# Kernel tuning notes

Hardware: AMD Instinct MI355X
Metric: run time of the kernel (lower is better)

The kernel has to match this reference:

```python
import jax, jax.numpy as jnp
import numpy as np

N = 40000      # num_ent
INIT = 100     # init_dim
D = 200        # gcn_dim
F = 4          # num_factors
E = 800000     # num edges (incl. inverses)
NREL = 800     # num_rel * 2
L = 2          # gcn_layer
B = 2048       # batch of (sub, rel)
H2 = D // 2    # CLUBSample hidden_size // 2
NPAIR = F * (F - 1) // 2  # 6 MI discriminators


def setup_inputs() -> dict:
    key = jax.random.key(0)
    ks = jax.random.split(key, 24)
    inp = {}
    inp['sub'] = jax.random.randint(ks[0], (B,), 0, N)
    inp['rel'] = jax.random.randint(ks[1], (B,), 0, NREL)
    inp['edge_index'] = jax.random.randint(ks[2], (2, E), 0, N)
    inp['edge_type'] = jax.random.randint(ks[3], (E,), 0, NREL)
    inp['perm'] = jax.random.permutation(ks[4], B)
    s = 0.05
    inp['init_embed'] = jax.random.normal(ks[5], (N, INIT), jnp.float32) * s
    inp['init_rel'] = jax.random.normal(ks[6], (NREL, D), jnp.float32) * s
    stdv = 1.0 / np.sqrt(F * D)
    inp['pca_w'] = jax.random.uniform(ks[7], (INIT, F * D), jnp.float32, -stdv, stdv)
    inp['pca_b'] = jax.random.uniform(ks[8], (F * D,), jnp.float32, -stdv, stdv)
    inp['cw_w'] = jax.random.normal(ks[9], (D, D), jnp.float32) * 0.1
    inp['w_rel'] = jax.random.normal(ks[10], (L, D, D), jnp.float32) * s
    # CLUBSample MLPs stacked over the NPAIR discriminators
    inp['mu_w1'] = jax.random.normal(ks[11], (NPAIR, D, H2), jnp.float32) * s
    inp['mu_b1'] = jnp.zeros((NPAIR, H2), jnp.float32)
    inp['mu_w2'] = jax.random.normal(ks[12], (NPAIR, H2, D), jnp.float32) * s
    inp['mu_b2'] = jnp.zeros((NPAIR, D), jnp.float32)
    inp['lv_w1'] = jax.random.normal(ks[13], (NPAIR, D, H2), jnp.float32) * s
    inp['lv_b1'] = jnp.zeros((NPAIR, H2), jnp.float32)
    inp['lv_w2'] = jax.random.normal(ks[14], (NPAIR, H2, D), jnp.float32) * s
    inp['lv_b2'] = jnp.zeros((NPAIR, D), jnp.float32)
    return inp


def _leaky(v):
    return jnp.where(v > 0, v, 0.2 * v)


def _club(xi, yj, yj_perm, w1, b1, w2, b2, v1, c1, v2, c2):
    # CLUBSample.forward: MI upper bound between factor i and factor j
    mu = jax.nn.relu(xi @ w1 + b1) @ w2 + b2
    logvar = jnp.tanh(jax.nn.relu(xi @ v1 + c1) @ v2 + c2)
    inv_var = jnp.exp(-logvar)
    pos = -(mu - yj) ** 2 * inv_var
    neg = -(mu - yj_perm) ** 2 * inv_var
    return (pos.sum(-1) - neg.sum(-1)).mean() / 2.0


def _encode(init_embed, init_rel, pca_w, pca_b, cw_w, w_rel, edge_index, edge_type):
    # SparseInputLinear + tanh -> [N, F, D]
    x = jnp.tanh(init_embed @ pca_w + pca_b).reshape(N, F, D)
    # CalculateWeight: leaky_relu matmul then softmax over the factor axis
    kw = _leaky(x.reshape(-1, D) @ cw_w).reshape(N, F, D)
    kw = jax.nn.softmax(kw, axis=1)
    r = init_rel
    src, dst = edge_index[0], edge_index[1]
    for l in range(L):
        r_edge = r[edge_type]  # [E, D]
        aggs = []
        for k in range(F):  # small fixed loop over factors to bound memory
            m = x[src, k] * r_edge                              # [E, D] messages
            logit = _leaky(jnp.sum(m * x[dst, k], axis=-1))     # [E] attention logits
            mx = jax.ops.segment_max(logit, dst, num_segments=N)
            a = jnp.exp(logit - mx[dst])
            den = jax.ops.segment_sum(a, dst, num_segments=N)
            a = a / (den[dst] + 1e-16)                          # per-dst softmax
            aggs.append(jax.ops.segment_sum(a[:, None] * m, dst, num_segments=N))
        agg = jnp.stack(aggs, axis=1)                           # [N, F, D]
        x = jnp.tanh(agg) * kw                                  # factor routing
        r = r @ w_rel[l]
    return x, r


def reference(sub, rel, edge_index, edge_type, perm,
              init_embed, init_rel, pca_w, pca_b, cw_w, w_rel,
              mu_w1, mu_b1, mu_w2, mu_b2, lv_w1, lv_b1, lv_w2, lv_b2):
    x, _ = _encode(init_embed, init_rel, pca_w, pca_b, cw_w, w_rel, edge_index, edge_type)
    sub_emb = x[sub].reshape(B, F * D)
    rel_emb = jnp.tile(init_rel[rel], (1, F))  # index_select + repeat(1, F)
    mi_loss = jnp.float32(0.0)
    cnt = 0
    for i in range(F):
        for j in range(i + 1, F):
            xi = sub_emb[:, i * D:(i + 1) * D]
            yj = sub_emb[:, j * D:(j + 1) * D]
            mi_loss = mi_loss + _club(xi, yj, yj[perm],
                                      mu_w1[cnt], mu_b1[cnt], mu_w2[cnt], mu_b2[cnt],
                                      lv_w1[cnt], lv_b1[cnt], lv_w2[cnt], lv_b2[cnt])
            cnt += 1
    return (sub_emb, rel_emb, x, mi_loss)
```

## Files before the change

kernel.cpp:

```cpp
#include <hip/hip_runtime.h>
#include <hip/hip_bf16.h>

#define N_NODES 40000
#define INIT_D  100
#define DD      200
#define FF      4
#define EE      800000
#define NRELS   800
#define BB      2048
#define H2D     100
#define FD      800
#define RPAD    224
#define XPAD    256

typedef __hip_bfloat16 bf16;
typedef unsigned char u8;
typedef unsigned short u16;
typedef unsigned int u32;
typedef float floatx2 __attribute__((ext_vector_type(2)));
typedef float floatx4 __attribute__((ext_vector_type(4)));
typedef u32 u32x2 __attribute__((ext_vector_type(2)));
typedef short bshort8 __attribute__((ext_vector_type(8)));

#define XSCALE 256.f
#define XINV   (1.f / 256.f)

__device__ __forceinline__ float b2f(bf16 v) { return __bfloat162float(v); }

__device__ __forceinline__ void fp8x4_dec(u32 q, float* o) {
    floatx2 lo = __builtin_amdgcn_cvt_pk_f32_fp8((int)q, false);
    floatx2 hi = __builtin_amdgcn_cvt_pk_f32_fp8((int)q, true);
    o[0] = lo.x; o[1] = lo.y; o[2] = hi.x; o[3] = hi.y;
}

__device__ __forceinline__ u32 fp8x4_enc(float v0, float v1, float v2, float v3) {
    int o = 0;
    o = __builtin_amdgcn_cvt_pk_fp8_f32(v0, v1, o, false);
    o = __builtin_amdgcn_cvt_pk_fp8_f32(v2, v3, o, true);
    return (u32)o;
}

__device__ __forceinline__ float red16(float v) {
    int t;
    t = __builtin_amdgcn_update_dpp(0, __float_as_int(v), 0xB1, 0xF, 0xF, true);
    v += __int_as_float(t);
    t = __builtin_amdgcn_update_dpp(0, __float_as_int(v), 0x4E, 0xF, 0xF, true);
    v += __int_as_float(t);
    t = __builtin_amdgcn_update_dpp(0, __float_as_int(v), 0x124, 0xF, 0xF, true);
    v += __int_as_float(t);
    t = __builtin_amdgcn_update_dpp(0, __float_as_int(v), 0x128, 0xF, 0xF, true);
    v += __int_as_float(t);
    return v;
}

__device__ __forceinline__ bshort8 fp8x8_bf16(u32x2 q) {
    float f[8];
    fp8x4_dec(q.x, f); fp8x4_dec(q.y, f + 4);
    bshort8 r;
#pragma unroll
    for (int j = 0; j < 8; j++) r[j] = (short)(__float_as_uint(f[j]) >> 16);
    return r;
}

__global__ __launch_bounds__(256) void zero_kernel(int* count, double* loss, u8* pad0, u8* pad1) {
    int idx = blockIdx.x * 256 + threadIdx.x;
    if (idx < N_NODES) count[idx] = 0;
    if (idx == 0) *loss = 0.0;
    if (idx < 64 && pad0) ((u32*)pad0)[idx] = 0u;
    if (idx < 64 && pad1) ((u32*)pad1)[idx] = 0u;
}

__global__ __launch_bounds__(64) void pca_kernel(const float* __restrict__ emb,
                                                 const float* __restrict__ pw,
                                                 const float* __restrict__ pb,
                                                 u8* __restrict__ xq,
                                                 float* __restrict__ xf,
                                                 int mode) {
    __shared__ float es[INIT_D][18];
    int r0 = blockIdx.y * 16;
    int c  = blockIdx.x * 64 + threadIdx.x;
    for (int idx = threadIdx.x; idx < 16 * INIT_D; idx += 64) {
        int r = idx / INIT_D, k = idx % INIT_D;
        es[k][r] = emb[(size_t)(r0 + r) * INIT_D + k];
    }
    __syncthreads();
    if (c >= FD) return;
    floatx2 acc[8];
#pragma unroll
    for (int i = 0; i < 8; i++) acc[i] = (floatx2){0.f, 0.f};
    for (int k = 0; k < INIT_D; k++) {
        float w = pw[k * FD + c];
        floatx2 w2 = (floatx2){w, w};
#pragma unroll
        for (int i = 0; i < 8; i++) acc[i] += *(const floatx2*)&es[k][2 * i] * w2;
    }
    float bias = pb[c];
#pragma unroll
    for (int r = 0; r < 16; r++) {
        float a = (r & 1) ? acc[r >> 1].y : acc[r >> 1].x;
        float v = tanhf(a + bias);
        if (mode == 0) {
            int t8 = __builtin_amdgcn_cvt_pk_fp8_f32(v * XSCALE, 0.f, 0, false);
            xq[(size_t)(r0 + r) * FD + c] = (u8)(t8 & 0xFF);
        } else {
            xf[(size_t)(r0 + r) * FD + c] = v;
        }
    }
}

__global__ __launch_bounds__(256) void bpack_kernel(const float* __restrict__ cw,
                                                    u16* __restrict__ bpH,
                                                    u16* __restrict__ bpL) {
    int w = (blockIdx.x * 256 + threadIdx.x) >> 6;
    int lane = threadIdx.x & 63;
    if (w >= 91) return;
    int t = w / 7, s = w % 7;
    int col = t * 16 + (lane & 15);
    int g = lane >> 4;
    bshort8 hv, lv;
#pragma unroll
    for (int j = 0; j < 8; j++) {
        int k = s * 32 + g * 8 + j;
        float v = (k < DD && col < DD) ? cw[k * DD + col] : 0.f;
        u32 b = __float_as_uint(v);
        u32 rb = b + 0x7FFFu + ((b >> 16) & 1u);
        u16 h = (u16)(rb >> 16);
        float hf = __uint_as_float(((u32)h) << 16);
        float lo = v - hf;
        u32 lb = __float_as_uint(lo);
        lb += 0x7FFFu + ((lb >> 16) & 1u);
        hv[j] = (short)h;
        lv[j] = (short)(lb >> 16);
    }
    size_t base = ((size_t)w * 64 + lane) * 8;
    *(bshort8*)(bpH + base) = hv;
    *(bshort8*)(bpL + base) = lv;
}

__global__ __launch_bounds__(256) void kw_mfma(const u8* __restrict__ xq,
                                               const u16* __restrict__ bpH,
                                               const u16* __restrict__ bpL,
                                               u8* __restrict__ kwout) {
    int wv = threadIdx.x >> 6, lane = threadIdx.x & 63;
    int Mbase = blockIdx.x * 128 + wv * 32;
    int g = lane >> 4, c16 = lane & 15;
    floatx4 acc[2][13];
#pragma unroll
    for (int m = 0; m < 2; m++)
#pragma unroll
        for (int t = 0; t < 13; t++) acc[m][t] = (floatx4){0.f, 0.f, 0.f, 0.f};

    const u8* a0p = xq + (size_t)(Mbase + c16) * DD + g * 8;
    const u8* a1p = a0p + 16 * DD;

    for (int s = 0; s < 7; s++) {
        u32x2 qa = *(const u32x2*)(a0p + s * 32);
        u32x2 qb = *(const u32x2*)(a1p + s * 32);
        bshort8 a0 = fp8x8_bf16(qa);
        bshort8 a1 = fp8x8_bf16(qb);
        const u16* hp = bpH + s * 512 + lane * 8;
        const u16* lp = bpL + s * 512 + lane * 8;
#pragma unroll
        for (int t = 0; t < 13; t++) {
            bshort8 bh = *(const bshort8*)(hp + (size_t)t * 3584);
            bshort8 bl = *(const bshort8*)(lp + (size_t)t * 3584);
            acc[0][t] = __builtin_amdgcn_mfma_f32_16x16x32_bf16(a0, bh, acc[0][t], 0, 0, 0);
            acc[1][t] = __builtin_amdgcn_mfma_f32_16x16x32_bf16(a1, bh, acc[1][t], 0, 0, 0);
            acc[0][t] = __builtin_amdgcn_mfma_f32_16x16x32_bf16(a0, bl, acc[0][t], 0, 0, 0);
            acc[1][t] = __builtin_amdgcn_mfma_f32_16x16x32_bf16(a1, bl, acc[1][t], 0, 0, 0);
        }
    }

    int rq = g * 4;
#pragma unroll
    for (int m = 0; m < 2; m++) {
#pragma unroll
        for (int t = 0; t < 13; t++) {
            int col = t * 16 + c16;
            if (col >= DD) continue;
            floatx4 a = acc[m][t];
            float v0 = a.x * XINV, v1 = a.y * XINV, v2 = a.z * XINV, v3 = a.w * XINV;
            v0 = v0 > 0.f ? v0 : 0.2f * v0;
            v1 = v1 > 0.f ? v1 : 0.2f * v1;
            v2 = v2 > 0.f ? v2 : 0.2f * v2;
            v3 = v3 > 0.f ? v3 : 0.2f * v3;
            float mx = fmaxf(fmaxf(v0, v1), fmaxf(v2, v3));
            float e0 = __expf(v0 - mx), e1 = __expf(v1 - mx);
            float e2 = __expf(v2 - mx), e3 = __expf(v3 - mx);
            float inv = 1.f / (e0 + e1 + e2 + e3);
            size_t base = (size_t)(Mbase + m * 16 + rq) * DD + col;
            kwout[base]           = (u8)(e0 * inv * 255.f + 0.5f);
            kwout[base + DD]      = (u8)(e1 * inv * 255.f + 0.5f);
            kwout[base + 2 * DD]  = (u8)(e2 * inv * 255.f + 0.5f);
            kwout[base + 3 * DD]  = (u8)(e3 * inv * 255.f + 0.5f);
        }
    }
}

__global__ __launch_bounds__(256) void kw_old(const float* __restrict__ x,
                                              const float* __restrict__ cw,
                                              u8* __restrict__ kw) {
    int wave = threadIdx.x >> 6, lane = threadIdx.x & 63;
    int n = blockIdx.x * 4 + wave;
    const float* xp = x + (size_t)n * FD;
    float acc[4][4];
#pragma unroll
    for (int f = 0; f < 4; f++)
#pragma unroll
        for (int i = 0; i < 4; i++) acc[f][i] = 0.f;
    for (int k = 0; k < DD; k++) {
        float xv0 = xp[k], xv1 = xp[DD + k];
        float xv2 = xp[2 * DD + k], xv3 = xp[3 * DD + k];
#pragma unroll
        for (int i = 0; i < 4; i++) {
            int d = i * 64 + lane;
            float w = (d < DD) ? cw[k * DD + d] : 0.f;
            acc[0][i] += xv0 * w; acc[1][i] += xv1 * w;
            acc[2][i] += xv2 * w; acc[3][i] += xv3 * w;
        }
    }
    u8* kwp = kw + (size_t)n * FD;
#pragma unroll
    for (int i = 0; i < 4; i++) {
        int d = i * 64 + lane;
        if (d >= DD) continue;
        float v0 = acc[0][i], v1 = acc[1][i], v2 = acc[2][i], v3 = acc[3][i];
        v0 = v0 > 0.f ? v0 : 0.2f * v0;
        v1 = v1 > 0.f ? v1 : 0.2f * v1;
        v2 = v2 > 0.f ? v2 : 0.2f * v2;
        v3 = v3 > 0.f ? v3 : 0.2f * v3;
        float m = fmaxf(fmaxf(v0, v1), fmaxf(v2, v3));
        float e0 = __expf(v0 - m), e1 = __expf(v1 - m), e2 = __expf(v2 - m), e3 = __expf(v3 - m);
        float inv = 1.f / (e0 + e1 + e2 + e3);
        kwp[d]          = (u8)(e0 * inv * 255.f + 0.5f);
        kwp[DD + d]     = (u8)(e1 * inv * 255.f + 0.5f);
        kwp[2 * DD + d] = (u8)(e2 * inv * 255.f + 0.5f);
        kwp[3 * DD + d] = (u8)(e3 * inv * 255.f + 0.5f);
    }
}

__global__ __launch_bounds__(256) void count_kernel(const int* __restrict__ dst, int* count) {
    int e = blockIdx.x * 256 + threadIdx.x;
    atomicAdd(&count[dst[e]], 1);
}

__global__ __launch_bounds__(1024) void scan_kernel(int* __restrict__ count, int* __restrict__ offs) {
    __shared__ int wsums[16];
    __shared__ int carry_s;
    int tid = threadIdx.x;
    int wv = tid >> 6, lane = tid & 63;
    if (tid == 0) { carry_s = 0; offs[0] = 0; }
    __syncthreads();
    for (int base = 0; base < 40960; base += 1024) {
        int i = base + tid;
        int v = (i < N_NODES) ? count[i] : 0;
        if (i < N_NODES) count[i] = 0;
        int x = v;
#pragma unroll
        for (int off = 1; off < 64; off <<= 1) {
            int y = __shfl_up(x, off, 64);
            if (lane >= off) x += y;
        }
        if (lane == 63) wsums[wv] = x;
        __syncthreads();
        if (wv == 0) {
            int s = (lane < 16) ? wsums[lane] : 0;
#pragma unroll
            for (int off = 1; off < 16; off <<= 1) {
                int y = __shfl_up(s, off, 64);
                if (lane >= off) s += y;
            }
            if (lane < 16) wsums[lane] = s;
        }
        __syncthreads();
        int add = carry_s + (wv > 0 ? wsums[wv - 1] : 0);
        int incl = x + add;
        if (i < N_NODES) offs[i + 1] = incl;
        __syncthreads();
        if (tid == 1023) carry_s = incl;
        __syncthreads();
    }
}

__global__ __launch_bounds__(256) void scatter_kernel(const int* __restrict__ src,
                                                      const int* __restrict__ dst,
                                                      const int* __restrict__ etyp,
                                                      const int* __restrict__ offs,
                                                      int* cursor,
                                                      u32* __restrict__ ep) {
    int e = blockIdx.x * 256 + threadIdx.x;
    int d = dst[e];
    int p = offs[d] + atomicAdd(&cursor[d], 1);
    ep[p] = ((u32)etyp[e] << 16) | (u32)src[e];
}

__global__ __launch_bounds__(256) void r0pad_kernel(const float* __restrict__ r0,
                                                    float* __restrict__ rp) {
    int idx = blockIdx.x * 256 + threadIdx.x;
    int n = idx / RPAD, d = idx % RPAD;
    rp[idx] = (d < DD) ? r0[n * DD + d] : 0.f;
}

__global__ __launch_bounds__(256) void rmul_kernel(const float* __restrict__ r0,
                                                   const float* __restrict__ w,
                                                   float* __restrict__ r1) {
    __shared__ float row[DD];
    int n = blockIdx.x;
    if (threadIdx.x < DD) row[threadIdx.x] = r0[n * DD + threadIdx.x];
    __syncthreads();
    int d = threadIdx.x;
    if (d < DD) {
        float acc = 0.f;
        for (int k = 0; k < DD; k++) acc += row[k] * w[k * DD + d];
        r1[n * RPAD + d] = acc;
    } else if (d < RPAD) {
        r1[n * RPAD + d] = 0.f;
    }
}

__global__ __launch_bounds__(256) void agg_fp8(const u8* __restrict__ xin,
                                               const u8* __restrict__ kwv,
                                               const float* __restrict__ r,
                                               const int* __restrict__ offs,
                                               const u32* __restrict__ ep,
                                               u8* __restrict__ xoq,
                                               float* __restrict__ xof,
                                               int mode) {
    int n    = blockIdx.x * 4 + (threadIdx.x >> 6);
    int lane = threadIdx.x & 63;
    int f    = lane >> 4;
    int k    = lane & 15;
    bool act = k < 13;
    int xoff = f * DD + k * 16;
    int roffc = k * 16; if (roffc > 200) roffc = 200;

    float xdf[16];
    {
        const u8* xdp = xin + (size_t)n * FD + xoff;
        u32x2 a = *(const u32x2*)xdp;
        u32x2 b = *(const u32x2*)(xdp + 8);
        fp8x4_dec(a.x, xdf); fp8x4_dec(a.y, xdf + 4);
        fp8x4_dec(b.x, xdf + 8); fp8x4_dec(b.y, xdf + 12);
    }
    floatx2 xd2[8];
#pragma unroll
    for (int j = 0; j < 8; j++) xd2[j] = (floatx2){xdf[2 * j], xdf[2 * j + 1]};

    floatx2 A[8];
#pragma unroll
    for (int j = 0; j < 8; j++) A[j] = (floatx2){0.f, 0.f};
    float Sm = 0.f;

    int e0 = offs[n], e1 = offs[n + 1];

#define ISSUE(QA, QB, R0, R1, R2, R3, JJ) do {                                  \
    u32 wrd_ = (u32)__builtin_amdgcn_readlane((int)epv, (JJ));                  \
    int s_ = (int)(wrd_ & 0xFFFFu), t_ = (int)(wrd_ >> 16);                     \
    const u8* xsp_ = xin + (size_t)s_ * FD;                                     \
    const float* rp_ = r + (size_t)t_ * RPAD + roffc;                           \
    QA = *(const u32x2*)(xsp_ + xoff);                                          \
    QB = *(const u32x2*)(xsp_ + xoff + 8);                                      \
    const floatx4* r4_ = (const floatx4*)rp_;                                   \
    R0 = r4_[0]; R1 = r4_[1]; R2 = r4_[2]; R3 = r4_[3];                         \
} while (0)

#define COMPUTE(QA, QB, R0, R1, R2, R3) do {                                    \
    float xsf_[16];                                                             \
    fp8x4_dec(QA.x, xsf_);     fp8x4_dec(QA.y, xsf_ + 4);                       \
    fp8x4_dec(QB.x, xsf_ + 8); fp8x4_dec(QB.y, xsf_ + 12);                      \
    floatx2 rr_[8];                                                             \
    rr_[0] = (floatx2){R0.x, R0.y}; rr_[1] = (floatx2){R0.z, R0.w};             \
    rr_[2] = (floatx2){R1.x, R1.y}; rr_[3] = (floatx2){R1.z, R1.w};             \
    rr_[4] = (floatx2){R2.x, R2.y}; rr_[5] = (floatx2){R2.z, R2.w};             \
    rr_[6] = (floatx2){R3.x, R3.y}; rr_[7] = (floatx2){R3.z, R3.w};             \
    floatx2 mm_[8];                                                             \
    floatx2 ps_ = (floatx2){0.f, 0.f};                                          \
    _Pragma("unroll")                                                           \
    for (int j_ = 0; j_ < 8; j_++) {                                            \
        floatx2 xs2_ = (floatx2){xsf_[2 * j_], xsf_[2 * j_ + 1]};               \
        mm_[j_] = xs2_ * rr_[j_];                                               \
        ps_ += mm_[j_] * xd2[j_];                                               \
    }                                                                           \
    float p_ = red16(ps_.x + ps_.y);                                            \
    float q_ = p_ * (XINV * XINV);                                              \
    float lg_ = fmaxf(q_, 0.2f * q_);                                           \
    float wg_ = __expf(lg_);                                                    \
    Sm += wg_;                                                                  \
    floatx2 w2_ = (floatx2){wg_, wg_};                                          \
    _Pragma("unroll")                                                           \
    for (int j_ = 0; j_ < 8; j_++) A[j_] += w2_ * mm_[j_];                      \
} while (0)

    for (int cb = e0; cb < e1; cb += 64) {
        int cnt = e1 - cb; if (cnt > 64) cnt = 64;
        u32 epv = ep[cb + (lane < cnt ? lane : cnt - 1)];
        u32x2 qaA, qbA, qaB, qbB;
        floatx4 rA0, rA1, rA2, rA3, rB0, rB1, rB2, rB3;
        ISSUE(qaA, qbA, rA0, rA1, rA2, rA3, 0);
        if (cnt > 1) ISSUE(qaB, qbB, rB0, rB1, rB2, rB3, 1);
        int m2 = cnt & ~1;
        for (int ii = 0; ii < m2; ii += 2) {
            COMPUTE(qaA, qbA, rA0, rA1, rA2, rA3);
            if (ii + 2 < cnt) ISSUE(qaA, qbA, rA0, rA1, rA2, rA3, ii + 2);
            COMPUTE(qaB, qbB, rB0, rB1, rB2, rB3);
            if (ii + 3 < cnt) ISSUE(qaB, qbB, rB0, rB1, rB2, rB3, ii + 3);
        }
        if (cnt & 1) COMPUTE(qaA, qbA, rA0, rA1, rA2, rA3);
    }
#undef ISSUE
#undef COMPUTE

    float inv = 1.f / (Sm + 1e-16f);
    u32 kws[4];
    {
        const u8* kwp = kwv + (size_t)n * FD + xoff;
        u32x2 ka = *(const u32x2*)kwp;
        u32x2 kb = *(const u32x2*)(kwp + 8);
        kws[0] = ka.x; kws[1] = ka.y; kws[2] = kb.x; kws[3] = kb.y;
    }
    float v[16];
#pragma unroll
    for (int j = 0; j < 16; j++) {
        float kv = (float)((kws[j >> 2] >> ((j & 3) * 8)) & 0xFF) * (1.f / 255.f);
        float Aj = (j & 1) ? A[j >> 1].y : A[j >> 1].x;
        v[j] = tanhf(Aj * inv * XINV) * kv;
    }
    if (mode == 0) {
        if (act) {
            u32 o0 = fp8x4_enc(v[0] * XSCALE, v[1] * XSCALE, v[2] * XSCALE, v[3] * XSCALE);
            u32 o1 = fp8x4_enc(v[4] * XSCALE, v[5] * XSCALE, v[6] * XSCALE, v[7] * XSCALE);
            u32 o2 = fp8x4_enc(v[8] * XSCALE, v[9] * XSCALE, v[10] * XSCALE, v[11] * XSCALE);
            u32 o3 = fp8x4_enc(v[12] * XSCALE, v[13] * XSCALE, v[14] * XSCALE, v[15] * XSCALE);
            u8* op = xoq + (size_t)n * FD + xoff;
            *(u32x2*)op = (u32x2){o0, o1};
            if (k < 12) *(u32x2*)(op + 8) = (u32x2){o2, o3};
        }
    } else {
        if (act) {
            float* op = xof + (size_t)n * FD + xoff;
            *(floatx4*)op       = (floatx4){v[0], v[1], v[2], v[3]};
            *(floatx4*)(op + 4) = (floatx4){v[4], v[5], v[6], v[7]};
            if (k < 12) {
                *(floatx4*)(op + 8)  = (floatx4){v[8], v[9], v[10], v[11]};
                *(floatx4*)(op + 12) = (floatx4){v[12], v[13], v[14], v[15]};
            }
        }
    }
}

__global__ __launch_bounds__(256) void agg_sliced(const float* __restrict__ xall,
                                                  const u8* __restrict__ kw,
                                                  const float* __restrict__ r,
                                                  const int* __restrict__ offs,
                                                  const u32* __restrict__ ep,
                                                  bf16* __restrict__ xtmp,
                                                  int f) {
    int n    = blockIdx.x * 4 + (threadIdx.x >> 6);
    int lane = threadIdx.x & 63;
    const float* xdp = xall + (size_t)n * FD + f * DD;
    float xd[4];
#pragma unroll
    for (int i = 0; i < 4; i++) {
        int d = i * 64 + lane;
        xd[i] = (d < DD) ? xdp[d] : 0.f;
    }
    float M = -INFINITY, S = 0.f;
    float A0 = 0.f, A1 = 0.f, A2 = 0.f, A3 = 0.f;
    int e0 = offs[n], e1 = offs[n + 1];
    for (int e = e0; e < e1; ++e) {
        u32 wrd = ep[e];
        int s = wrd & 0xFFFF, t = wrd >> 16;
        const float* xsp = xall + (size_t)s * FD + f * DD;
        const float* rp = r + (size_t)t * RPAD;
        float mm[4];
        float p = 0.f;
#pragma unroll
        for (int i = 0; i < 4; i++) {
            int d = i * 64 + lane;
            float xs = (d < DD) ? xsp[d] : 0.f;
            float rrv = (d < DD) ? rp[d] : 0.f;
            mm[i] = xs * rrv;
            p += mm[i] * xd[i];
        }
#pragma unroll
        for (int o = 32; o > 0; o >>= 1) p += __shfl_xor(p, o, 64);
        float logit = p > 0.f ? p : 0.2f * p;
        float nm = fmaxf(M, logit);
        float sc = __expf(M - nm);
        float w  = __expf(logit - nm);
        S  = S * sc + w;
        A0 = A0 * sc + w * mm[0];
        A1 = A1 * sc + w * mm[1];
        A2 = A2 * sc + w * mm[2];
        A3 = A3 * sc + w * mm[3];
        M = nm;
    }
    float inv = 1.f / (S + 1e-16f);
    const u8* kwp = kw + (size_t)n * FD + f * DD;
    bf16* xo = xtmp + (size_t)n * DD;
    float A[4] = {A0, A1, A2, A3};
#pragma unroll
    for (int i = 0; i < 4; i++) {
        int d = i * 64 + lane;
        if (d < DD) {
            float kv = (float)kwp[d] * (1.f / 255.f);
            xo[d] = __float2bfloat16(tanhf(A[i] * inv) * kv);
        }
    }
}

__global__ __launch_bounds__(256) void copyback_kernel(const bf16* __restrict__ xtmp,
                                                       float* __restrict__ xall, int f) {
    int idx = blockIdx.x * 256 + threadIdx.x;
    int n = idx / DD, d = idx % DD;
    xall[(size_t)n * FD + f * DD + d] = b2f(xtmp[idx]);
}

__global__ __launch_bounds__(256) void subemb_kernel(const float* __restrict__ x,
                                                     const int* __restrict__ sub,
                                                     float* __restrict__ out) {
    int idx = blockIdx.x * 256 + threadIdx.x;
    int b = idx / FD, c = idx % FD;
    out[idx] = x[(size_t)sub[b] * FD + c];
}

__global__ __launch_bounds__(256) void relemb_kernel(const float* __restrict__ ir,
                                                     const int* __restrict__ rel,
                                                     float* __restrict__ out) {
    int idx = blockIdx.x * 256 + threadIdx.x;
    int b = idx / FD, d = idx % DD;
    out[idx] = ir[(size_t)rel[b] * DD + d];
}

__global__ __launch_bounds__(256) void club_kernel(const float* __restrict__ se,
                                                   const int* __restrict__ perm,
                                                   const float* __restrict__ mu_w1, const float* __restrict__ mu_b1,
                                                   const float* __restrict__ mu_w2, const float* __restrict__ mu_b2,
                                                   const float* __restrict__ lv_w1, const float* __restrict__ lv_b1,
                                                   const float* __restrict__ lv_w2, const float* __restrict__ lv_b2,
                                                   double* loss) {
    const int PI[6] = {0, 0, 0, 1, 1, 2};
    const int PJ[6] = {1, 2, 3, 2, 3, 3};
    int p = blockIdx.y;
    int i = PI[p], j = PJ[p];
    __shared__ float xi[DD], yj[DD], yjp[DD], h1m[H2D], h1v[H2D];
    __shared__ float wsum[4];
    float psum = 0.f;
    for (int rr = 0; rr < 8; ++rr) {
        int b = blockIdx.x * 8 + rr;
        int bp = perm[b];
        if (threadIdx.x < DD) {
            int t = threadIdx.x;
            xi[t]  = se[(size_t)b * FD + i * DD + t];
            yj[t]  = se[(size_t)b * FD + j * DD + t];
            yjp[t] = se[(size_t)bp * FD + j * DD + t];
        }
        __syncthreads();
        if (threadIdx.x < H2D) {
            int c = threadIdx.x;
            float a1 = mu_b1[p * H2D + c];
            float a2 = lv_b1[p * H2D + c];
            for (int d = 0; d < DD; d++) {
                float xv = xi[d];
                a1 += xv * mu_w1[(size_t)p * DD * H2D + d * H2D + c];
                a2 += xv * lv_w1[(size_t)p * DD * H2D + d * H2D + c];
            }
            h1m[c] = fmaxf(a1, 0.f);
            h1v[c] = fmaxf(a2, 0.f);
        }
        __syncthreads();
        if (threadIdx.x < DD) {
            int d = threadIdx.x;
            float m = mu_b2[p * DD + d];
            float v = lv_b2[p * DD + d];
            for (int c = 0; c < H2D; c++) {
                m += h1m[c] * mu_w2[(size_t)p * H2D * DD + c * DD + d];
                v += h1v[c] * lv_w2[(size_t)p * H2D * DD + c * DD + d];
            }
            float lv = tanhf(v);
            float ivr = __expf(-lv);
            float d1 = m - yj[d], d2 = m - yjp[d];
            psum += (d2 * d2 - d1 * d1) * ivr;
        }
        __syncthreads();
    }
    float v = psum;
#pragma unroll
    for (int o = 32; o > 0; o >>= 1) v += __shfl_xor(v, o, 64);
    if ((threadIdx.x & 63) == 0) wsum[threadIdx.x >> 6] = v;
    __syncthreads();
    if (threadIdx.x == 0) {
        double t = (double)wsum[0] + (double)wsum[1] + (double)wsum[2] + (double)wsum[3];
        atomicAdd(loss, t / (2.0 * (double)BB));
    }
}

__global__ void loss_out_kernel(const double* loss, float* out) {
    if (threadIdx.x == 0 && blockIdx.x == 0)
        out[0] = (float)(*loss);
}

extern "C" void kernel_launch(void* const* d_in, const int* in_sizes, int n_in,
                              void* d_out, int out_size, void* d_ws, size_t ws_size,
                              hipStream_t stream) {
    const int* sub  = (const int*)d_in[0];
    const int* rel  = (const int*)d_in[1];
    const int* eidx = (const int*)d_in[2];
    const int* etyp = (const int*)d_in[3];
    const int* perm = (const int*)d_in[4];
    const float* init_embed = (const float*)d_in[5];
    const float* init_rel   = (const float*)d_in[6];
    const float* pca_w = (const float*)d_in[7];
    const float* pca_b = (const float*)d_in[8];
    const float* cw_w  = (const float*)d_in[9];
    const float* w_rel = (const float*)d_in[10];
    const float* mu_w1 = (const float*)d_in[11];
    const float* mu_b1 = (const float*)d_in[12];
    const float* mu_w2 = (const float*)d_in[13];
    const float* mu_b2 = (const float*)d_in[14];
    const float* lv_w1 = (const float*)d_in[15];
    const float* lv_b1 = (const float*)d_in[16];
    const float* lv_w2 = (const float*)d_in[17];
    const float* lv_b2 = (const float*)d_in[18];

    float* out = (float*)d_out;
    const size_t OFF_SUB = 0;
    const size_t OFF_REL = 1638400;
    const size_t OFF_X   = 3276800;
    const size_t OFF_MI  = 35276800;
    float* xall = out + OFF_X;

    const int* src = eidx;
    const int* dst = eidx + EE;

    bool fast = (ws_size >= (size_t)101 * 1000 * 1000);

    char* w = (char*)d_ws;
    u8* xq0 = nullptr; u8* xq1 = nullptr; bf16* xtmp = nullptr;
    if (fast) {
        xq0 = (u8*)w; w += (size_t)N_NODES * FD + XPAD;
        xq1 = (u8*)w; w += (size_t)N_NODES * FD + XPAD;
    } else {
        xtmp = (bf16*)w; w += (size_t)N_NODES * DD * 2;
    }
    u8*   kwb  = (u8*)w;    w += (size_t)N_NODES * FD + XPAD;
    float* r0p = (float*)w; w += NRELS * RPAD * 4;
    float* r1  = (float*)w; w += NRELS * RPAD * 4;
    u32* ep    = (u32*)w;   w += EE * 4;
    int* count = (int*)w;   w += N_NODES * 4;
    int* offs  = (int*)w;   w += (N_NODES + 16) * 4;
    double* loss = (double*)w; w += 256;

    u16* bpH = (u16*)ep;
    u16* bpL = bpH + 13 * 7 * 64 * 8;

    hipLaunchKernelGGL(zero_kernel, dim3(157), dim3(256), 0, stream, count, loss,
                       fast ? xq0 + (size_t)N_NODES * FD : nullptr,
                       fast ? xq1 + (size_t)N_NODES * FD : nullptr);
    if (fast) hipLaunchKernelGGL(bpack_kernel, dim3(23), dim3(256), 0, stream, cw_w, bpH, bpL);
    hipLaunchKernelGGL(pca_kernel, dim3(13, 2500), dim3(64), 0, stream,
                       init_embed, pca_w, pca_b, xq0, xall, fast ? 0 : 1);
    if (fast) hipLaunchKernelGGL(kw_mfma, dim3(1250), dim3(256), 0, stream, xq0, bpH, bpL, kwb);
    else      hipLaunchKernelGGL(kw_old, dim3(10000), dim3(256), 0, stream, xall, cw_w, kwb);
    hipLaunchKernelGGL(count_kernel, dim3(3125), dim3(256), 0, stream, dst, count);
    hipLaunchKernelGGL(scan_kernel, dim3(1), dim3(1024), 0, stream, count, offs);
    hipLaunchKernelGGL(scatter_kernel, dim3(3125), dim3(256), 0, stream, src, dst, etyp, offs, count, ep);
    hipLaunchKernelGGL(r0pad_kernel, dim3(700), dim3(256), 0, stream, init_rel, r0p);
    hipLaunchKernelGGL(rmul_kernel, dim3(800), dim3(256), 0, stream, init_rel, w_rel, r1);

    if (fast) {
        hipLaunchKernelGGL(agg_fp8, dim3(10000), dim3(256), 0, stream,
                           xq0, kwb, r0p, offs, ep, xq1, (float*)nullptr, 0);
        hipLaunchKernelGGL(agg_fp8, dim3(10000), dim3(256), 0, stream,
                           xq1, kwb, r1, offs, ep, (u8*)nullptr, xall, 1);
    } else {
        for (int f = 0; f < FF; f++) {
            hipLaunchKernelGGL(agg_sliced, dim3(10000), dim3(256), 0, stream,
                               xall, kwb, r0p, offs, ep, xtmp, f);
            hipLaunchKernelGGL(copyback_kernel, dim3(31250), dim3(256), 0, stream, xtmp, xall, f);
        }
        for (int f = 0; f < FF; f++) {
            hipLaunchKernelGGL(agg_sliced, dim3(10000), dim3(256), 0, stream,
                               xall, kwb, r1, offs, ep, xtmp, f);
            hipLaunchKernelGGL(copyback_kernel, dim3(31250), dim3(256), 0, stream, xtmp, xall, f);
        }
    }

    hipLaunchKernelGGL(subemb_kernel, dim3(6400), dim3(256), 0, stream, xall, sub, out + OFF_SUB);
    hipLaunchKernelGGL(relemb_kernel, dim3(6400), dim3(256), 0, stream, init_rel, rel, out + OFF_REL);
    hipLaunchKernelGGL(club_kernel, dim3(256, 6), dim3(256), 0, stream, out + OFF_SUB, perm,
                       mu_w1, mu_b1, mu_w2, mu_b2, lv_w1, lv_b1, lv_w2, lv_b2, loss);
    hipLaunchKernelGGL(loss_out_kernel, dim3(1), dim3(64), 0, stream, loss, out + OFF_MI);
}
```

Before: 1.215 ms.

## Sort nodes by degree, stage B in LDS, deepen agg pipeline, rebalance CLUB

After: 1.412 ms. 16.2% more time.

```diff
diff --git a/kernel.cpp b/kernel.cpp
--- a/kernel.cpp
+++ b/kernel.cpp
@@ -62,12 +62,14 @@
     return r;
 }
 
-__global__ __launch_bounds__(256) void zero_kernel(int* count, double* loss, u8* pad0, u8* pad1) {
+__global__ __launch_bounds__(256) void zero_kernel(int* count, double* loss, u8* pad0, u8* pad1,
+                                                   int* bins, int* bcur) {
     int idx = blockIdx.x * 256 + threadIdx.x;
     if (idx < N_NODES) count[idx] = 0;
     if (idx == 0) *loss = 0.0;
     if (idx < 64 && pad0) ((u32*)pad0)[idx] = 0u;
     if (idx < 64 && pad1) ((u32*)pad1)[idx] = 0u;
+    if (idx < 256 && bins) { bins[idx] = 0; bcur[idx] = 0; }
 }
 
 __global__ __launch_bounds__(64) void pca_kernel(const float* __restrict__ emb,
@@ -109,8 +111,7 @@
 }
 
 __global__ __launch_bounds__(256) void bpack_kernel(const float* __restrict__ cw,
-                                                    u16* __restrict__ bpH,
-                                                    u16* __restrict__ bpL) {
+                                                    u16* __restrict__ bp) {
     int w = (blockIdx.x * 256 + threadIdx.x) >> 6;
     int lane = threadIdx.x & 63;
     if (w >= 91) return;
@@ -132,15 +133,15 @@
         hv[j] = (short)h;
         lv[j] = (short)(lb >> 16);
     }
-    size_t base = ((size_t)w * 64 + lane) * 8;
-    *(bshort8*)(bpH + base) = hv;
-    *(bshort8*)(bpL + base) = lv;
+    size_t base = ((size_t)((s * 13 + t) * 2) * 64 + lane) * 8;
+    *(bshort8*)(bp + base) = hv;
+    *(bshort8*)(bp + base + 512) = lv;
 }
 
 __global__ __launch_bounds__(256) void kw_mfma(const u8* __restrict__ xq,
-                                               const u16* __restrict__ bpH,
-                                               const u16* __restrict__ bpL,
+                                               const u16* __restrict__ bp,
                                                u8* __restrict__ kwout) {
+    __shared__ u16 bs[13312];
     int wv = threadIdx.x >> 6, lane = threadIdx.x & 63;
     int Mbase = blockIdx.x * 128 + wv * 32;
     int g = lane >> 4, c16 = lane & 15;
@@ -152,18 +153,26 @@
 
     const u8* a0p = xq + (size_t)(Mbase + c16) * DD + g * 8;
     const u8* a1p = a0p + 16 * DD;
+    u32x2 qa = *(const u32x2*)a0p;
+    u32x2 qb = *(const u32x2*)a1p;
 
     for (int s = 0; s < 7; s++) {
-        u32x2 qa = *(const u32x2*)(a0p + s * 32);
-        u32x2 qb = *(const u32x2*)(a1p + s * 32);
+        __syncthreads();
+        const floatx4* gs = (const floatx4*)(bp + (size_t)s * 13312);
+        floatx4* ld = (floatx4*)bs;
+        for (int i = threadIdx.x; i < 1664; i += 256) ld[i] = gs[i];
+        __syncthreads();
         bshort8 a0 = fp8x8_bf16(qa);
         bshort8 a1 = fp8x8_bf16(qb);
-        const u16* hp = bpH + s * 512 + lane * 8;
-        const u16* lp = bpL + s * 512 + lane * 8;
+        if (s < 6) {
+            qa = *(const u32x2*)(a0p + (s + 1) * 32);
+            qb = *(const u32x2*)(a1p + (s + 1) * 32);
+        }
 #pragma unroll
         for (int t = 0; t < 13; t++) {
-            bshort8 bh = *(const bshort8*)(hp + (size_t)t * 3584);
-            bshort8 bl = *(const bshort8*)(lp + (size_t)t * 3584);
+            const u16* tb = bs + t * 1024;
+            bshort8 bh = *(const bshort8*)(tb + lane * 8);
+            bshort8 bl = *(const bshort8*)(tb + 512 + lane * 8);
             acc[0][t] = __builtin_amdgcn_mfma_f32_16x16x32_bf16(a0, bh, acc[0][t], 0, 0, 0);
             acc[1][t] = __builtin_amdgcn_mfma_f32_16x16x32_bf16(a1, bh, acc[1][t], 0, 0, 0);
             acc[0][t] = __builtin_amdgcn_mfma_f32_16x16x32_bf16(a0, bl, acc[0][t], 0, 0, 0);
@@ -294,6 +303,50 @@
     ep[p] = ((u32)etyp[e] << 16) | (u32)src[e];
 }
 
+__global__ __launch_bounds__(256) void deg_hist(const int* __restrict__ offs, int* bins) {
+    int n = blockIdx.x * 256 + threadIdx.x;
+    if (n < N_NODES) {
+        int d = offs[n + 1] - offs[n];
+        if (d > 255) d = 255;
+        atomicAdd(&bins[d], 1);
+    }
+}
+
+__global__ __launch_bounds__(256) void bin_scan(const int* __restrict__ bins, int* __restrict__ bstart) {
+    __shared__ int ws[4];
+    __shared__ int tot;
+    int tid = threadIdx.x, wv = tid >> 6, lane = tid & 63;
+    int x = bins[tid];
+#pragma unroll
+    for (int off = 1; off < 64; off <<= 1) {
+        int y = __shfl_up(x, off, 64);
+        if (lane >= off) x += y;
+    }
+    if (lane == 63) ws[wv] = x;
+    __syncthreads();
+    int add = 0;
+    if (wv > 0) add += ws[0];
+    if (wv > 1) add += ws[1];
+    if (wv > 2) add += ws[2];
+    int incl = x + add;
+    if (tid == 255) tot = incl;
+    __syncthreads();
+    bstart[tid] = tot - incl;
+}
+
+__global__ __launch_bounds__(256) void order_scatter(const int* __restrict__ offs,
+                                                     const int* __restrict__ bstart,
+                                                     int* bcur,
+                                                     int* __restrict__ order) {
+    int n = blockIdx.x * 256 + threadIdx.x;
+    if (n < N_NODES) {
+        int d = offs[n + 1] - offs[n];
+        if (d > 255) d = 255;
+        int pos = bstart[d] + atomicAdd(&bcur[d], 1);
+        order[pos] = n;
+    }
+}
+
 __global__ __launch_bounds__(256) void r0pad_kernel(const float* __restrict__ r0,
                                                     float* __restrict__ rp) {
     int idx = blockIdx.x * 256 + threadIdx.x;
@@ -323,10 +376,11 @@
                                                const float* __restrict__ r,
                                                const int* __restrict__ offs,
                                                const u32* __restrict__ ep,
+                                               const int* __restrict__ order,
                                                u8* __restrict__ xoq,
                                                float* __restrict__ xof,
                                                int mode) {
-    int n    = blockIdx.x * 4 + (threadIdx.x >> 6);
+    int n    = order[blockIdx.x * 4 + (threadIdx.x >> 6)];
     int lane = threadIdx.x & 63;
     int f    = lane >> 4;
     int k    = lane & 15;
@@ -394,18 +448,21 @@
     for (int cb = e0; cb < e1; cb += 64) {
         int cnt = e1 - cb; if (cnt > 64) cnt = 64;
         u32 epv = ep[cb + (lane < cnt ? lane : cnt - 1)];
-        u32x2 qaA, qbA, qaB, qbB;
-        floatx4 rA0, rA1, rA2, rA3, rB0, rB1, rB2, rB3;
+        u32x2 qaA, qbA, qaB, qbB, qaC, qbC;
+        floatx4 rA0, rA1, rA2, rA3, rB0, rB1, rB2, rB3, rC0, rC1, rC2, rC3;
         ISSUE(qaA, qbA, rA0, rA1, rA2, rA3, 0);
         if (cnt > 1) ISSUE(qaB, qbB, rB0, rB1, rB2, rB3, 1);
-        int m2 = cnt & ~1;
-        for (int ii = 0; ii < m2; ii += 2) {
+        if (cnt > 2) ISSUE(qaC, qbC, rC0, rC1, rC2, rC3, 2);
+        for (int ii = 0; ii < cnt; ii += 3) {
             COMPUTE(qaA, qbA, rA0, rA1, rA2, rA3);
-            if (ii + 2 < cnt) ISSUE(qaA, qbA, rA0, rA1, rA2, rA3, ii + 2);
+            if (ii + 3 < cnt) ISSUE(qaA, qbA, rA0, rA1, rA2, rA3, ii + 3);
+            if (ii + 1 >= cnt) break;
             COMPUTE(qaB, qbB, rB0, rB1, rB2, rB3);
-            if (ii + 3 < cnt) ISSUE(qaB, qbB, rB0, rB1, rB2, rB3, ii + 3);
-        }
-        if (cnt & 1) COMPUTE(qaA, qbA, rA0, rA1, rA2, rA3);
+            if (ii + 4 < cnt) ISSUE(qaB, qbB, rB0, rB1, rB2, rB3, ii + 4);
+            if (ii + 2 >= cnt) break;
+            COMPUTE(qaC, qbC, rC0, rC1, rC2, rC3);
+            if (ii + 5 < cnt) ISSUE(qaC, qbC, rC0, rC1, rC2, rC3, ii + 5);
+        }
     }
 #undef ISSUE
 #undef COMPUTE
@@ -438,11 +495,15 @@
     } else {
         if (act) {
             float* op = xof + (size_t)n * FD + xoff;
-            *(floatx4*)op       = (floatx4){v[0], v[1], v[2], v[3]};
-            *(floatx4*)(op + 4) = (floatx4){v[4], v[5], v[6], v[7]};
+            floatx4 w0 = (floatx4){v[0], v[1], v[2], v[3]};
+            floatx4 w1 = (floatx4){v[4], v[5], v[6], v[7]};
+            __builtin_nontemporal_store(w0, (floatx4*)op);
+            __builtin_nontemporal_store(w1, (floatx4*)(op + 4));
             if (k < 12) {
-                *(floatx4*)(op + 8)  = (floatx4){v[8], v[9], v[10], v[11]};
-                *(floatx4*)(op + 12) = (floatx4){v[12], v[13], v[14], v[15]};
+                floatx4 w2 = (floatx4){v[8], v[9], v[10], v[11]};
+                floatx4 w3 = (floatx4){v[12], v[13], v[14], v[15]};
+                __builtin_nontemporal_store(w2, (floatx4*)(op + 8));
+                __builtin_nontemporal_store(w3, (floatx4*)(op + 12));
             }
         }
     }
@@ -546,31 +607,32 @@
     __shared__ float xi[DD], yj[DD], yjp[DD], h1m[H2D], h1v[H2D];
     __shared__ float wsum[4];
     float psum = 0.f;
-    for (int rr = 0; rr < 8; ++rr) {
-        int b = blockIdx.x * 8 + rr;
+    int tid = threadIdx.x;
+    for (int rr = 0; rr < 2; ++rr) {
+        int b = blockIdx.x * 2 + rr;
         int bp = perm[b];
-        if (threadIdx.x < DD) {
-            int t = threadIdx.x;
-            xi[t]  = se[(size_t)b * FD + i * DD + t];
-            yj[t]  = se[(size_t)b * FD + j * DD + t];
-            yjp[t] = se[(size_t)bp * FD + j * DD + t];
-        }
-        __syncthreads();
-        if (threadIdx.x < H2D) {
-            int c = threadIdx.x;
+        if (tid < DD) {
+            xi[tid]  = se[(size_t)b * FD + i * DD + tid];
+            yj[tid]  = se[(size_t)b * FD + j * DD + tid];
+            yjp[tid] = se[(size_t)bp * FD + j * DD + tid];
+        }
+        __syncthreads();
+        if (tid < H2D) {
+            int c = tid;
             float a1 = mu_b1[p * H2D + c];
+            for (int d = 0; d < DD; d++)
+                a1 += xi[d] * mu_w1[(size_t)p * DD * H2D + d * H2D + c];
+            h1m[c] = fmaxf(a1, 0.f);
+        } else if (tid >= 128 && tid < 128 + H2D) {
+            int c = tid - 128;
             float a2 = lv_b1[p * H2D + c];
-            for (int d = 0; d < DD; d++) {
-                float xv = xi[d];
-                a1 += xv * mu_w1[(size_t)p * DD * H2D + d * H2D + c];
-                a2 += xv * lv_w1[(size_t)p * DD * H2D + d * H2D + c];
-            }
-            h1m[c] = fmaxf(a1, 0.f);
+            for (int d = 0; d < DD; d++)
+                a2 += xi[d] * lv_w1[(size_t)p * DD * H2D + d * H2D + c];
             h1v[c] = fmaxf(a2, 0.f);
         }
         __syncthreads();
-        if (threadIdx.x < DD) {
-            int d = threadIdx.x;
+        if (tid < DD) {
+            int d = tid;
             float m = mu_b2[p * DD + d];
             float v = lv_b2[p * DD + d];
             for (int c = 0; c < H2D; c++) {
@@ -587,9 +649,9 @@
     float v = psum;
 #pragma unroll
     for (int o = 32; o > 0; o >>= 1) v += __shfl_xor(v, o, 64);
-    if ((threadIdx.x & 63) == 0) wsum[threadIdx.x >> 6] = v;
+    if ((tid & 63) == 0) wsum[tid >> 6] = v;
     __syncthreads();
-    if (threadIdx.x == 0) {
+    if (tid == 0) {
         double t = (double)wsum[0] + (double)wsum[1] + (double)wsum[2] + (double)wsum[3];
         atomicAdd(loss, t / (2.0 * (double)BB));
     }
@@ -651,28 +713,38 @@
     int* offs  = (int*)w;   w += (N_NODES + 16) * 4;
     double* loss = (double*)w; w += 256;
 
-    u16* bpH = (u16*)ep;
-    u16* bpL = bpH + 13 * 7 * 64 * 8;
+    u16* bp = (u16*)ep;
+
+    int* order  = (int*)(out + OFF_REL);
+    int* bins   = order + 40960;
+    int* bstart = bins + 256;
+    int* bcur   = bstart + 256;
 
     hipLaunchKernelGGL(zero_kernel, dim3(157), dim3(256), 0, stream, count, loss,
                        fast ? xq0 + (size_t)N_NODES * FD : nullptr,
-                       fast ? xq1 + (size_t)N_NODES * FD : nullptr);
-    if (fast) hipLaunchKernelGGL(bpack_kernel, dim3(23), dim3(256), 0, stream, cw_w, bpH, bpL);
+                       fast ? xq1 + (size_t)N_NODES * FD : nullptr,
+                       fast ? bins : nullptr, fast ? bcur : nullptr);
+    if (fast) hipLaunchKernelGGL(bpack_kernel, dim3(23), dim3(256), 0, stream, cw_w, bp);
     hipLaunchKernelGGL(pca_kernel, dim3(13, 2500), dim3(64), 0, stream,
                        init_embed, pca_w, pca_b, xq0, xall, fast ? 0 : 1);
-    if (fast) hipLaunchKernelGGL(kw_mfma, dim3(1250), dim3(256), 0, stream, xq0, bpH, bpL, kwb);
+    if (fast) hipLaunchKernelGGL(kw_mfma, dim3(1250), dim3(256), 0, stream, xq0, bp, kwb);
     else      hipLaunchKernelGGL(kw_old, dim3(10000), dim3(256), 0, stream, xall, cw_w, kwb);
     hipLaunchKernelGGL(count_kernel, dim3(3125), dim3(256), 0, stream, dst, count);
     hipLaunchKernelGGL(scan_kernel, dim3(1), dim3(1024), 0, stream, count, offs);
     hipLaunchKernelGGL(scatter_kernel, dim3(3125), dim3(256), 0, stream, src, dst, etyp, offs, count, ep);
+    if (fast) {
+        hipLaunchKernelGGL(deg_hist, dim3(157), dim3(256), 0, stream, offs, bins);
+        hipLaunchKernelGGL(bin_scan, dim3(1), dim3(256), 0, stream, bins, bstart);
+        hipLaunchKernelGGL(order_scatter, dim3(157), dim3(256), 0, stream, offs, bstart, bcur, order);
+    }
     hipLaunchKernelGGL(r0pad_kernel, dim3(700), dim3(256), 0, stream, init_rel, r0p);
     hipLaunchKernelGGL(rmul_kernel, dim3(800), dim3(256), 0, stream, init_rel, w_rel, r1);
 
     if (fast) {
         hipLaunchKernelGGL(agg_fp8, dim3(10000), dim3(256), 0, stream,
-                           xq0, kwb, r0p, offs, ep, xq1, (float*)nullptr, 0);
+                           xq0, kwb, r0p, offs, ep, order, xq1, (float*)nullptr, 0);
         hipLaunchKernelGGL(agg_fp8, dim3(10000), dim3(256), 0, stream,
-                           xq1, kwb, r1, offs, ep, (u8*)nullptr, xall, 1);
+                           xq1, kwb, r1, offs, ep, order, (u8*)nullptr, xall, 1);
     } else {
         for (int f = 0; f < FF; f++) {
             hipLaunchKernelGGL(agg_sliced, dim3(10000), dim3(256), 0, stream,
@@ -688,7 +760,7 @@
 
     hipLaunchKernelGGL(subemb_kernel, dim3(6400), dim3(256), 0, stream, xall, sub, out + OFF_SUB);
     hipLaunchKernelGGL(relemb_kernel, dim3(6400), dim3(256), 0, stream, init_rel, rel, out + OFF_REL);
-    hipLaunchKernelGGL(club_kernel, dim3(256, 6), dim3(256), 0, stream, out + OFF_SUB, perm,
+    hipLaunchKernelGGL(club_kernel, dim3(1024, 6), dim3(256), 0, stream, out + OFF_SUB, perm,
                        mu_w1, mu_b1, mu_w2, mu_b2, lv_w1, lv_b1, lv_w2, lv_b2, loss);
     hipLaunchKernelGGL(loss_out_kernel, dim3(1), dim3(64), 0, stream, loss, out + OFF_MI);
 }
```

## Stage kw weights in LDS, raise agg occupancy, widen CLUB grid

Applied to the files above, without the earlier changes.

New measurement: 4.588 ms. 3.78x slower.

```diff
diff --git a/kernel.cpp b/kernel.cpp
--- a/kernel.cpp
+++ b/kernel.cpp
@@ -109,8 +109,7 @@
 }
 
 __global__ __launch_bounds__(256) void bpack_kernel(const float* __restrict__ cw,
-                                                    u16* __restrict__ bpH,
-                                                    u16* __restrict__ bpL) {
+                                                    u16* __restrict__ bp) {
     int w = (blockIdx.x * 256 + threadIdx.x) >> 6;
     int lane = threadIdx.x & 63;
     if (w >= 91) return;
@@ -132,15 +131,15 @@
         hv[j] = (short)h;
         lv[j] = (short)(lb >> 16);
     }
-    size_t base = ((size_t)w * 64 + lane) * 8;
-    *(bshort8*)(bpH + base) = hv;
-    *(bshort8*)(bpL + base) = lv;
+    size_t base = ((size_t)((s * 13 + t) * 2) * 64 + lane) * 8;
+    *(bshort8*)(bp + base) = hv;
+    *(bshort8*)(bp + base + 512) = lv;
 }
 
 __global__ __launch_bounds__(256) void kw_mfma(const u8* __restrict__ xq,
-                                               const u16* __restrict__ bpH,
-                                               const u16* __restrict__ bpL,
+                                               const u16* __restrict__ bp,
                                                u8* __restrict__ kwout) {
+    __shared__ u16 bs[13312];
     int wv = threadIdx.x >> 6, lane = threadIdx.x & 63;
     int Mbase = blockIdx.x * 128 + wv * 32;
     int g = lane >> 4, c16 = lane & 15;
@@ -152,18 +151,26 @@
 
     const u8* a0p = xq + (size_t)(Mbase + c16) * DD + g * 8;
     const u8* a1p = a0p + 16 * DD;
+    u32x2 qa = *(const u32x2*)a0p;
+    u32x2 qb = *(const u32x2*)a1p;
 
     for (int s = 0; s < 7; s++) {
-        u32x2 qa = *(const u32x2*)(a0p + s * 32);
-        u32x2 qb = *(const u32x2*)(a1p + s * 32);
+        __syncthreads();
+        const floatx4* gs = (const floatx4*)(bp + (size_t)s * 13312);
+        floatx4* ld = (floatx4*)bs;
+        for (int i = threadIdx.x; i < 1664; i += 256) ld[i] = gs[i];
+        __syncthreads();
         bshort8 a0 = fp8x8_bf16(qa);
         bshort8 a1 = fp8x8_bf16(qb);
-        const u16* hp = bpH + s * 512 + lane * 8;
-        const u16* lp = bpL + s * 512 + lane * 8;
+        if (s < 6) {
+            qa = *(const u32x2*)(a0p + (s + 1) * 32);
+            qb = *(const u32x2*)(a1p + (s + 1) * 32);
+        }
 #pragma unroll
         for (int t = 0; t < 13; t++) {
-            bshort8 bh = *(const bshort8*)(hp + (size_t)t * 3584);
-            bshort8 bl = *(const bshort8*)(lp + (size_t)t * 3584);
+            const u16* tb = bs + t * 1024;
+            bshort8 bh = *(const bshort8*)(tb + lane * 8);
+            bshort8 bl = *(const bshort8*)(tb + 512 + lane * 8);
             acc[0][t] = __builtin_amdgcn_mfma_f32_16x16x32_bf16(a0, bh, acc[0][t], 0, 0, 0);
             acc[1][t] = __builtin_amdgcn_mfma_f32_16x16x32_bf16(a1, bh, acc[1][t], 0, 0, 0);
             acc[0][t] = __builtin_amdgcn_mfma_f32_16x16x32_bf16(a0, bl, acc[0][t], 0, 0, 0);
@@ -318,14 +325,14 @@
     }
 }
 
-__global__ __launch_bounds__(256) void agg_fp8(const u8* __restrict__ xin,
-                                               const u8* __restrict__ kwv,
-                                               const float* __restrict__ r,
-                                               const int* __restrict__ offs,
-                                               const u32* __restrict__ ep,
-                                               u8* __restrict__ xoq,
-                                               float* __restrict__ xof,
-                                               int mode) {
+__global__ __launch_bounds__(256, 8) void agg_fp8(const u8* __restrict__ xin,
+                                                  const u8* __restrict__ kwv,
+                                                  const float* __restrict__ r,
+                                                  const int* __restrict__ offs,
+                                                  const u32* __restrict__ ep,
+                                                  u8* __restrict__ xoq,
+                                                  float* __restrict__ xof,
+                                                  int mode) {
     int n    = blockIdx.x * 4 + (threadIdx.x >> 6);
     int lane = threadIdx.x & 63;
     int f    = lane >> 4;
@@ -546,31 +553,32 @@
     __shared__ float xi[DD], yj[DD], yjp[DD], h1m[H2D], h1v[H2D];
     __shared__ float wsum[4];
     float psum = 0.f;
-    for (int rr = 0; rr < 8; ++rr) {
-        int b = blockIdx.x * 8 + rr;
+    int tid = threadIdx.x;
+    for (int rr = 0; rr < 2; ++rr) {
+        int b = blockIdx.x * 2 + rr;
         int bp = perm[b];
-        if (threadIdx.x < DD) {
-            int t = threadIdx.x;
-            xi[t]  = se[(size_t)b * FD + i * DD + t];
-            yj[t]  = se[(size_t)b * FD + j * DD + t];
-            yjp[t] = se[(size_t)bp * FD + j * DD + t];
-        }
-        __syncthreads();
-        if (threadIdx.x < H2D) {
-            int c = threadIdx.x;
+        if (tid < DD) {
+            xi[tid]  = se[(size_t)b * FD + i * DD + tid];
+            yj[tid]  = se[(size_t)b * FD + j * DD + tid];
+            yjp[tid] = se[(size_t)bp * FD + j * DD + tid];
+        }
+        __syncthreads();
+        if (tid < H2D) {
+            int c = tid;
             float a1 = mu_b1[p * H2D + c];
+            for (int d = 0; d < DD; d++)
+                a1 += xi[d] * mu_w1[(size_t)p * DD * H2D + d * H2D + c];
+            h1m[c] = fmaxf(a1, 0.f);
+        } else if (tid >= 128 && tid < 128 + H2D) {
+            int c = tid - 128;
             float a2 = lv_b1[p * H2D + c];
-            for (int d = 0; d < DD; d++) {
-                float xv = xi[d];
-                a1 += xv * mu_w1[(size_t)p * DD * H2D + d * H2D + c];
-                a2 += xv * lv_w1[(size_t)p * DD * H2D + d * H2D + c];
-            }
-            h1m[c] = fmaxf(a1, 0.f);
+            for (int d = 0; d < DD; d++)
+                a2 += xi[d] * lv_w1[(size_t)p * DD * H2D + d * H2D + c];
             h1v[c] = fmaxf(a2, 0.f);
         }
         __syncthreads();
-        if (threadIdx.x < DD) {
-            int d = threadIdx.x;
+        if (tid < DD) {
+            int d = tid;
             float m = mu_b2[p * DD + d];
             float v = lv_b2[p * DD + d];
             for (int c = 0; c < H2D; c++) {
@@ -587,9 +595,9 @@
     float v = psum;
 #pragma unroll
     for (int o = 32; o > 0; o >>= 1) v += __shfl_xor(v, o, 64);
-    if ((threadIdx.x & 63) == 0) wsum[threadIdx.x >> 6] = v;
+    if ((tid & 63) == 0) wsum[tid >> 6] = v;
     __syncthreads();
-    if (threadIdx.x == 0) {
+    if (tid == 0) {
         double t = (double)wsum[0] + (double)wsum[1] + (double)wsum[2] + (double)wsum[3];
         atomicAdd(loss, t / (2.0 * (double)BB));
     }
@@ -651,16 +659,15 @@
     int* offs  = (int*)w;   w += (N_NODES + 16) * 4;
     double* loss = (double*)w; w += 256;
 
-    u16* bpH = (u16*)ep;
-    u16* bpL = bpH + 13 * 7 * 64 * 8;
+    u16* bp = (u16*)ep;
 
     hipLaunchKernelGGL(zero_kernel, dim3(157), dim3(256), 0, stream, count, loss,
                        fast ? xq0 + (size_t)N_NODES * FD : nullptr,
                        fast ? xq1 + (size_t)N_NODES * FD : nullptr);
-    if (fast) hipLaunchKernelGGL(bpack_kernel, dim3(23), dim3(256), 0, stream, cw_w, bpH, bpL);
+    if (fast) hipLaunchKernelGGL(bpack_kernel, dim3(23), dim3(256), 0, stream, cw_w, bp);
     hipLaunchKernelGGL(pca_kernel, dim3(13, 2500), dim3(64), 0, stream,
                        init_embed, pca_w, pca_b, xq0, xall, fast ? 0 : 1);
-    if (fast) hipLaunchKernelGGL(kw_mfma, dim3(1250), dim3(256), 0, stream, xq0, bpH, bpL, kwb);
+    if (fast) hipLaunchKernelGGL(kw_mfma, dim3(1250), dim3(256), 0, stream, xq0, bp, kwb);
     else      hipLaunchKernelGGL(kw_old, dim3(10000), dim3(256), 0, stream, xall, cw_w, kwb);
     hipLaunchKernelGGL(count_kernel, dim3(3125), dim3(256), 0, stream, dst, count);
     hipLaunchKernelGGL(scan_kernel, dim3(1), dim3(1024), 0, stream, count, offs);
@@ -688,7 +695,7 @@
 
     hipLaunchKernelGGL(subemb_kernel, dim3(6400), dim3(256), 0, stream, xall, sub, out + OFF_SUB);
     hipLaunchKernelGGL(relemb_kernel, dim3(6400), dim3(256), 0, stream, init_rel, rel, out + OFF_REL);
-    hipLaunchKernelGGL(club_kernel, dim3(256, 6), dim3(256), 0, stream, out + OFF_SUB, perm,
+    hipLaunchKernelGGL(club_kernel, dim3(1024, 6), dim3(256), 0, stream, out + OFF_SUB, perm,
                        mu_w1, mu_b1, mu_w2, mu_b2, lv_w1, lv_b1, lv_w2, lv_b2, loss);
     hipLaunchKernelGGL(loss_out_kernel, dim3(1), dim3(64), 0, stream, loss, out + OFF_MI);
 }
```
